# Performance work log

Measured on AMD Instinct MI355X. Metric: run time of the kernel, lower is better.

## Reference

```python
import jax, jax.numpy as jnp
import numpy as np

B, IN, O, F, FH = 512, 2000, 64, 8, 32
D = 64 + FH * O  # 2112


def setup_inputs() -> dict:
    key = jax.random.key(0)
    ks = jax.random.split(key, 17)
    rn = lambda k, s: jax.random.normal(k, s, dtype=jnp.float32) * 0.05
    return dict(
        x=rn(ks[0], (B, IN)),
        fc_in_W=rn(ks[1], (1024, IN)), fc_in_b=rn(ks[2], (1024,)),
        fc1_W=rn(ks[3], (128, 1024)), fc1_b=rn(ks[4], (128,)),
        out1_W=rn(ks[5], (O, 64, 128)), out1_b=rn(ks[6], (O, 64)),
        coef_nn_W=rn(ks[7], (F, FH, 1)), coef_nn_b=rn(ks[8], (F, FH)),
        coef_att_W=rn(ks[9], (F, FH, FH)),
        out_att_W=rn(ks[10], (O, FH, FH)),
        nodes_trans_W=rn(ks[11], (O, O)),
        trans_gcn_W=rn(ks[12], (D, D)),
        outmap_W=rn(ks[13], (1, D)), outmap_b=rn(ks[14], (1,)),
        prelu_a=jnp.float32(0.25),
        coef_m=rn(ks[15], (O, O, F)),
    )


def reference(x, fc_in_W, fc_in_b, fc1_W, fc1_b, out1_W, out1_b,
              coef_nn_W, coef_nn_b, coef_att_W, out_att_W,
              nodes_trans_W, trans_gcn_W, outmap_W, outmap_b, prelu_a, coef_m):
    elu = jax.nn.elu
    # trunk MLP
    h = jax.nn.relu(x @ fc_in_W.T + fc_in_b)          # [B,1024]
    h = jax.nn.relu(h @ fc1_W.T + fc1_b)              # [B,128]
    # per-output-node heads (vectorized over the output_dim loop)
    hiddens = jax.nn.relu(jnp.einsum('bk,odk->bod', h, out1_W) + out1_b)  # [B,O,64]
    # per-feature coef embedding: Linear(1,FH) on each coef_m[:,:,i] slice
    cf = elu(coef_m[..., None] * coef_nn_W[:, :, 0] + coef_nn_b)          # [O,O,F,FH]
    # sum over concatenated feature axis (F*FH) of exp(elu(.))
    s = jnp.exp(elu(cf)).sum(axis=(2, 3))[:, :, None, None]               # [O,O,1,1]
    lin = jnp.einsum('xyfh,fgh->xyfg', cf, coef_att_W)                    # per-feature attention linear
    p = elu(jnp.exp(elu(cf)) * lin / s)
    cfs = elu(p.sum(axis=2) / F)                                          # [O,O,FH]
    # node-level attention (vectorized over the output_dim loop)
    coef_sum = jnp.exp(elu(cfs)).sum(axis=1)                              # [O,FH]
    p2 = jnp.exp(elu(cfs)) / coef_sum[:, None, :]                         # [O,O,FH]
    lin2 = jnp.einsum('oih,igh->oig', cfs, out_att_W)
    att = (p2 * lin2).reshape(O, O * FH)                                  # concat over i (i-major)
    hc = jnp.concatenate(
        [hiddens, jnp.broadcast_to(att[None], (x.shape[0], O, O * FH))], axis=2)  # [B,O,D]
    nt = jnp.einsum('bpd,op->bod', hc, nodes_trans_W)                     # node mixing Linear(O,O)
    trans = jax.nn.sigmoid(jnp.einsum('bod,ed->boe', nt, trans_gcn_W))    # [B,O,D]
    z = (trans @ outmap_W.T + outmap_b).squeeze(-1)                       # [B,O]
    return jnp.where(z >= 0, z, prelu_a * z)                              # PReLU
```

## Files before the change

### kernel.cpp

```cpp
#include <hip/hip_runtime.h>
#include <math.h>

typedef __attribute__((ext_vector_type(8))) short bf16x8;
typedef __attribute__((ext_vector_type(4))) float f32x4;

static __device__ __forceinline__ float fast_elu(float x) {
    return x > 0.0f ? x : __expf(x) - 1.0f;
}

static __device__ __forceinline__ unsigned short f2bf(float f) {
    unsigned int u = __float_as_uint(f);
    unsigned int r = (u + 0x7FFFu + ((u >> 16) & 1u)) >> 16;
    return (unsigned short)r;
}

#define CV0 1048576
#define CV1 3145728
#define CV2 3276800
#define CV3 3280896
#define CV4 3805184
#define CV5 8265728
__global__ __launch_bounds__(256) void conv_all(
    const float* __restrict__ x, const float* __restrict__ fcinW,
    const float* __restrict__ fc1W, const float* __restrict__ ntW,
    const float* __restrict__ out1W, const float* __restrict__ tgw,
    unsigned short* __restrict__ xb, unsigned short* __restrict__ fcinWb,
    unsigned short* __restrict__ fc1Wb, unsigned short* __restrict__ Wb,
    unsigned short* __restrict__ out1WbT,
    unsigned short* __restrict__ Gb, unsigned short* __restrict__ G2b)
{
    int idx = blockIdx.x * 256 + threadIdx.x;
    if (idx < CV0) {
        int r = idx >> 11, k = idx & 2047;
        xb[idx] = (k < 2000) ? f2bf(x[(size_t)r * 2000 + k]) : (unsigned short)0;
    } else if (idx < CV1) {
        int i = idx - CV0;
        int r = i >> 11, k = i & 2047;
        fcinWb[i] = (k < 2000) ? f2bf(fcinW[(size_t)r * 2000 + k]) : (unsigned short)0;
    } else if (idx < CV2) {
        int i = idx - CV1;
        fc1Wb[i] = f2bf(fc1W[i]);
    } else if (idx < CV3) {
        int i = idx - CV2;
        Wb[i] = f2bf(ntW[i]);
    } else if (idx < CV4) {
        int i = idx - CV3;
        int n = i >> 7, k = i & 127, d = n >> 6, p = n & 63;
        out1WbT[i] = f2bf(out1W[(size_t)((p << 6) | d) * 128 + k]);
    } else if (idx < CV5) {
        int i = idx - CV4;
        int e = i / 2112, k = i - e * 2112;
        unsigned short v = f2bf(tgw[(size_t)e * 2112 + k]);
        if (k < 64) Gb[e * 64 + k] = v;
        else        G2b[(size_t)e * 2048 + (k - 64)] = v;
    }
}

__global__ __launch_bounds__(256) void gemm_mfma(
    const unsigned short* __restrict__ A, int lda,
    const unsigned short* __restrict__ B, int ldb,
    float* __restrict__ C, unsigned short* __restrict__ Cb,
    int ldc, long strideCz,
    const float* __restrict__ bias, int mode, int kchunk)
{
    __shared__ __align__(16) unsigned short As[64 * 40];
    __shared__ __align__(16) unsigned short Bs[64 * 40];
    const int t = threadIdx.x;
    const int w = t >> 6, lane = t & 63, l16 = lane & 15, quad = lane >> 4;
    const int n0 = blockIdx.x * 64, m0 = blockIdx.y * 64;
    const int kb0 = blockIdx.z * kchunk;
    const int r = t >> 2, koff = (t & 3) * 8;
    if (mode == 0) C += (size_t)blockIdx.z * strideCz;

    const size_t arow = (size_t)(m0 + r) * lda + koff;
    const size_t brow = (size_t)(n0 + r) * ldb + koff;
    bf16x8 av = *reinterpret_cast<const bf16x8*>(&A[arow + kb0]);
    bf16x8 bv = *reinterpret_cast<const bf16x8*>(&B[brow + kb0]);

    f32x4 acc[4] = {};
    for (int kb = kb0; kb < kb0 + kchunk; kb += 32) {
        __syncthreads();
        *reinterpret_cast<bf16x8*>(&As[r * 40 + koff]) = av;
        *reinterpret_cast<bf16x8*>(&Bs[r * 40 + koff]) = bv;
        if (kb + 32 < kb0 + kchunk) {
            av = *reinterpret_cast<const bf16x8*>(&A[arow + kb + 32]);
            bv = *reinterpret_cast<const bf16x8*>(&B[brow + kb + 32]);
        }
        __syncthreads();
        bf16x8 af = *reinterpret_cast<const bf16x8*>(&As[(w * 16 + l16) * 40 + quad * 8]);
        #pragma unroll
        for (int nt = 0; nt < 4; ++nt) {
            bf16x8 bf = *reinterpret_cast<const bf16x8*>(&Bs[(nt * 16 + l16) * 40 + quad * 8]);
            acc[nt] = __builtin_amdgcn_mfma_f32_16x16x32_bf16(af, bf, acc[nt], 0, 0, 0);
        }
    }
    #pragma unroll
    for (int nt = 0; nt < 4; ++nt)
        #pragma unroll
        for (int i = 0; i < 4; ++i) {
            int m = m0 + w * 16 + quad * 4 + i;
            int n = n0 + nt * 16 + l16;
            if (mode == 0) {
                C[(size_t)m * ldc + n] = acc[nt][i];
            } else {
                int bidx = (((n & 63) << 6) | (n >> 6));
                float v = acc[nt][i] + bias[bidx];
                v = fmaxf(v, 0.0f);
                Cb[(size_t)m * ldc + n] = f2bf(v);
            }
        }
}

__global__ __launch_bounds__(256) void reduce_partials(
    const float* __restrict__ src, float* __restrict__ dstF,
    unsigned short* __restrict__ dstB, int n,
    int nparts, long pstride, const float* __restrict__ bias, int biasMask, int doRelu)
{
    int i = blockIdx.x * 256 + threadIdx.x;
    if (i >= n) return;
    float a = 0.0f;
    for (int j = 0; j < nparts; ++j) a += src[i + (long)j * pstride];
    if (bias) a += bias[i & biasMask];
    if (doRelu) a = fmaxf(a, 0.0f);
    if (dstB) dstB[i] = f2bf(a); else dstF[i] = a;
}

__global__ __launch_bounds__(256) void coef_kernel(
    const float* __restrict__ coef_m,
    const float* __restrict__ cW,
    const float* __restrict__ cB,
    const float* __restrict__ attW,
    float* __restrict__ cfs)
{
    __shared__ float cf_s[4][256];
    __shared__ float part[4][64];
    const int t = threadIdx.x;
    const int wv = t >> 6, lane = t & 63;
    const int xy = blockIdx.x * 4 + wv;
    float ls = 0.0f;
    #pragma unroll
    for (int i = 0; i < 4; ++i) {
        int idx = i * 64 + lane;
        int f = idx >> 5;
        float v = fast_elu(coef_m[xy * 8 + f] * cW[idx] + cB[idx]);
        cf_s[wv][idx] = v;
        ls += __expf(fast_elu(v));
    }
    #pragma unroll
    for (int m = 1; m < 64; m <<= 1) ls += __shfl_xor(ls, m, 64);
    __syncthreads();
    const float rs = __builtin_amdgcn_rcpf(ls);
    const int g = lane & 31, fg = lane >> 5;
    float acc = 0.0f;
    for (int f = fg * 4; f < fg * 4 + 4; ++f) {
        float lin = 0.0f;
        #pragma unroll
        for (int h = 0; h < 32; h += 4) {
            float4 Lv = *reinterpret_cast<const float4*>(&cf_s[wv][f * 32 + h]);
            float4 Wv = *reinterpret_cast<const float4*>(&attW[f * 1024 + g * 32 + h]);
            lin += Lv.x * Wv.x + Lv.y * Wv.y + Lv.z * Wv.z + Lv.w * Wv.w;
        }
        float e = __expf(fast_elu(cf_s[wv][f * 32 + g]));
        acc += fast_elu(e * lin * rs);
    }
    part[wv][lane] = acc;
    __syncthreads();
    if (lane < 32) {
        float tot = part[wv][lane] + part[wv][lane + 32];
        cfs[xy * 32 + lane] = fast_elu(tot * 0.125f);
    }
}

__global__ __launch_bounds__(1024) void att_kernel(
    const float* __restrict__ cfs,
    const float* __restrict__ oattW,
    float* __restrict__ att)
{
    __shared__ float L[2048];
    __shared__ float red[1024];
    __shared__ float csum[32];
    const int t = threadIdx.x;
    const int o = blockIdx.x;
    L[t] = cfs[o * 2048 + t];
    L[t + 1024] = cfs[o * 2048 + 1024 + t];
    __syncthreads();
    {
        int h = t & 31, ig = t >> 5;
        red[t] = __expf(fast_elu(L[(2 * ig) * 32 + h])) +
                 __expf(fast_elu(L[(2 * ig + 1) * 32 + h]));
        __syncthreads();
        if (t < 32) {
            float cs = 0.0f;
            #pragma unroll
            for (int j = 0; j < 32; ++j) cs += red[j * 32 + t];
            csum[t] = cs;
        }
        __syncthreads();
    }
    #pragma unroll
    for (int j = 0; j < 2; ++j) {
        int idx = t + 1024 * j;
        int i = idx >> 5, g = idx & 31;
        float lin2 = 0.0f;
        #pragma unroll
        for (int h = 0; h < 32; h += 4) {
            float4 Lv = *reinterpret_cast<const float4*>(&L[i * 32 + h]);
            float4 Wv = *reinterpret_cast<const float4*>(&oattW[i * 1024 + g * 32 + h]);
            lin2 += Lv.x * Wv.x + Lv.y * Wv.y + Lv.z * Wv.z + Lv.w * Wv.w;
        }
        float p2 = __expf(fast_elu(L[idx])) * __builtin_amdgcn_rcpf(csum[g]);
        att[o * 2048 + idx] = p2 * lin2;
    }
}

__global__ __launch_bounds__(256) void natt_new(
    const float* __restrict__ ntW,
    const float* __restrict__ att,
    unsigned short* __restrict__ nattb)
{
    __shared__ float ntW_s[64 * 65];
    __shared__ float att_s[64 * 17];
    const int t = threadIdx.x;
    const int d0 = blockIdx.x * 16;
    #pragma unroll
    for (int j = 0; j < 16; ++j) {
        int idx = t + 256 * j;
        ntW_s[(idx >> 6) * 65 + (idx & 63)] = ntW[idx];
    }
    #pragma unroll
    for (int j = 0; j < 4; ++j) {
        int idx = t + 256 * j;
        int p = idx >> 4, dd = idx & 15;
        att_s[p * 17 + dd] = att[p * 2048 + d0 + dd];
    }
    __syncthreads();
    const int dd = t & 15, ob = (t >> 4) * 4;
    float acc[4] = {0.0f, 0.0f, 0.0f, 0.0f};
    for (int p = 0; p < 64; ++p) {
        float av = att_s[p * 17 + dd];
        #pragma unroll
        for (int i = 0; i < 4; ++i) acc[i] += ntW_s[(ob + i) * 65 + p] * av;
    }
    #pragma unroll
    for (int i = 0; i < 4; ++i)
        nattb[(ob + i) * 2048 + d0 + dd] = f2bf(acc[i]);
}

__global__ __launch_bounds__(256) void final_part(
    const unsigned short* __restrict__ hbT,
    const unsigned short* __restrict__ Wb,
    const unsigned short* __restrict__ Gb,
    const float* __restrict__ cmatT,
    const float* __restrict__ outW,
    float* __restrict__ zpart)
{
    __shared__ __align__(16) unsigned short HtT[64 * 72];
    __shared__ __align__(16) unsigned short nt1_s[64 * 72];
    __shared__ float zp[4][64];
    const int t = threadIdx.x;
    const int w = t >> 6;
    const int lane = t & 63;
    const int l16 = lane & 15, quad = lane >> 4;
    const int b = blockIdx.x;
    const int z = blockIdx.y;

    const unsigned short* src = hbT + (size_t)b * 4096;
    #pragma unroll
    for (int j = 0; j < 2; ++j) {
        int c = t + j * 256;
        *reinterpret_cast<bf16x8*>(&HtT[(c >> 3) * 72 + (c & 7) * 8]) =
            *reinterpret_cast<const bf16x8*>(&src[c * 8]);
    }
    __syncthreads();

    bf16x8 aW[2];
    #pragma unroll
    for (int h = 0; h < 2; ++h)
        aW[h] = *reinterpret_cast<const bf16x8*>(&Wb[(w * 16 + l16) * 64 + h * 32 + quad * 8]);
    #pragma unroll
    for (int dt = 0; dt < 4; ++dt) {
        f32x4 acc = {0.0f, 0.0f, 0.0f, 0.0f};
        #pragma unroll
        for (int h = 0; h < 2; ++h) {
            bf16x8 bf = *reinterpret_cast<const bf16x8*>(
                &HtT[(dt * 16 + l16) * 72 + h * 32 + quad * 8]);
            acc = __builtin_amdgcn_mfma_f32_16x16x32_bf16(aW[h], bf, acc, 0, 0, 0);
        }
        #pragma unroll
        for (int i = 0; i < 4; ++i)
            nt1_s[(w * 16 + quad * 4 + i) * 72 + dt * 16 + l16] = f2bf(acc[i]);
    }
    __syncthreads();

    bf16x8 afr[4][2];
    #pragma unroll
    for (int ot = 0; ot < 4; ++ot)
        #pragma unroll
        for (int h = 0; h < 2; ++h)
            afr[ot][h] = *reinterpret_cast<const bf16x8*>(
                &nt1_s[(ot * 16 + l16) * 72 + h * 32 + quad * 8]);

    float zacc[4][4] = {};
    int e = z * 64 + w * 16 + l16;
    bf16x8 g0 = *reinterpret_cast<const bf16x8*>(&Gb[(size_t)e * 64 + quad * 8]);
    bf16x8 g1 = *reinterpret_cast<const bf16x8*>(&Gb[(size_t)e * 64 + 32 + quad * 8]);
    float wv = outW[e];
    float4 c4[4];
    #pragma unroll
    for (int ot = 0; ot < 4; ++ot)
        c4[ot] = *reinterpret_cast<const float4*>(&cmatT[(size_t)e * 64 + ot * 16 + quad * 4]);

    for (int ec = z; ec < 33; ec += 4) {
        const int en = e + 256;
        const bool more = (ec + 4 < 33);
        bf16x8 ng0, ng1; float4 nc4[4]; float nwv;
        if (more) {
            ng0 = *reinterpret_cast<const bf16x8*>(&Gb[(size_t)en * 64 + quad * 8]);
            ng1 = *reinterpret_cast<const bf16x8*>(&Gb[(size_t)en * 64 + 32 + quad * 8]);
            nwv = outW[en];
            #pragma unroll
            for (int ot = 0; ot < 4; ++ot)
                nc4[ot] = *reinterpret_cast<const float4*>(
                    &cmatT[(size_t)en * 64 + ot * 16 + quad * 4]);
        }
        #pragma unroll
        for (int ot = 0; ot < 4; ++ot) {
            f32x4 acc = {c4[ot].x, c4[ot].y, c4[ot].z, c4[ot].w};
            acc = __builtin_amdgcn_mfma_f32_16x16x32_bf16(afr[ot][0], g0, acc, 0, 0, 0);
            acc = __builtin_amdgcn_mfma_f32_16x16x32_bf16(afr[ot][1], g1, acc, 0, 0, 0);
            #pragma unroll
            for (int i = 0; i < 4; ++i) {
                float sg = __builtin_amdgcn_rcpf(1.0f + __expf(-acc[i]));
                zacc[ot][i] += sg * wv;
            }
        }
        if (more) {
            g0 = ng0; g1 = ng1; wv = nwv;
            #pragma unroll
            for (int ot = 0; ot < 4; ++ot) c4[ot] = nc4[ot];
        }
        e = en;
    }
    #pragma unroll
    for (int m = 1; m < 16; m <<= 1)
        #pragma unroll
        for (int ot = 0; ot < 4; ++ot)
            #pragma unroll
            for (int i = 0; i < 4; ++i)
                zacc[ot][i] += __shfl_xor(zacc[ot][i], m, 64);

    if (l16 == 0) {
        #pragma unroll
        for (int ot = 0; ot < 4; ++ot)
            #pragma unroll
            for (int i = 0; i < 4; ++i)
                zp[w][ot * 16 + quad * 4 + i] = zacc[ot][i];
    }
    __syncthreads();
    if (t < 64)
        zpart[((size_t)z * 512 + b) * 64 + t] = zp[0][t] + zp[1][t] + zp[2][t] + zp[3][t];
}

__global__ __launch_bounds__(256) void finish_kernel(
    const float* __restrict__ zpart, const float* __restrict__ outB,
    const float* __restrict__ preluA, float* __restrict__ out)
{
    int i = blockIdx.x * 256 + threadIdx.x;
    float z = zpart[i] + zpart[32768 + i] + zpart[65536 + i] + zpart[98304 + i] + outB[0];
    float pa = preluA[0];
    out[i] = (z >= 0.0f) ? z : pa * z;
}

extern "C" void kernel_launch(void* const* d_in, const int* in_sizes, int n_in,
                              void* d_out, int out_size, void* d_ws, size_t ws_size,
                              hipStream_t stream)
{
    const float* x       = (const float*)d_in[0];
    const float* fc_in_W = (const float*)d_in[1];
    const float* fc_in_b = (const float*)d_in[2];
    const float* fc1_W   = (const float*)d_in[3];
    const float* fc1_b   = (const float*)d_in[4];
    const float* out1_W  = (const float*)d_in[5];
    const float* out1_b  = (const float*)d_in[6];
    const float* cW      = (const float*)d_in[7];
    const float* cB      = (const float*)d_in[8];
    const float* cattW   = (const float*)d_in[9];
    const float* oattW   = (const float*)d_in[10];
    const float* ntW     = (const float*)d_in[11];
    const float* tgw     = (const float*)d_in[12];
    const float* outW    = (const float*)d_in[13];
    const float* outB    = (const float*)d_in[14];
    const float* preluA  = (const float*)d_in[15];
    const float* coef_m  = (const float*)d_in[16];
    float* out = (float*)d_out;
    float* ws  = (float*)d_ws;

    unsigned short* xb      = (unsigned short*)(ws + 0);
    unsigned short* fcinWb  = (unsigned short*)(ws + 524288);
    float*          cpT     = ws + 0;
    float*          h1p     = ws + 1572864;
    unsigned short* hbT     = (unsigned short*)(ws + 1572864);
    unsigned short* h1b     = (unsigned short*)(ws + 3670016);
    unsigned short* fc1Wb   = (unsigned short*)(ws + 3932160);
    float*          h2p     = ws + 3997696;
    float*          zpart   = ws + 3997696;
    unsigned short* h2b     = (unsigned short*)(ws + 4521984);
    unsigned short* out1WbT = (unsigned short*)(ws + 4554752);
    unsigned short* Wb      = (unsigned short*)(ws + 4816896);
    unsigned short* Gb      = (unsigned short*)(ws + 4818944);
    unsigned short* G2b     = (unsigned short*)(ws + 4886528);
    float*          cfs     = ws + 7049216;
    float*          att     = ws + 7180288;
    unsigned short* nattb   = (unsigned short*)(ws + 7311360);
    float*          cmatT   = ws + 7376896;

    conv_all<<<(CV5 + 255) / 256, 256, 0, stream>>>(
        x, fc_in_W, fc1_W, ntW, out1_W, tgw,
        xb, fcinWb, fc1Wb, Wb, out1WbT, Gb, G2b);

    coef_kernel<<<1024, 256, 0, stream>>>(coef_m, cW, cB, cattW, cfs);
    att_kernel<<<64, 1024, 0, stream>>>(cfs, oattW, att);
    natt_new<<<128, 256, 0, stream>>>(ntW, att, nattb);

    gemm_mfma<<<dim3(16, 8, 4), 256, 0, stream>>>(xb, 2048, fcinWb, 2048,
        h1p, nullptr, 1024, 524288L, nullptr, 0, 512);
    reduce_partials<<<2048, 256, 0, stream>>>(h1p, nullptr, h1b, 524288, 4,
        524288L, fc_in_b, 1023, 1);
    gemm_mfma<<<dim3(2, 8, 8), 256, 0, stream>>>(h1b, 1024, fc1Wb, 1024,
        h2p, nullptr, 128, 65536L, nullptr, 0, 128);
    reduce_partials<<<256, 256, 0, stream>>>(h2p, nullptr, h2b, 65536, 8,
        65536L, fc1_b, 127, 1);
    gemm_mfma<<<dim3(64, 8, 1), 256, 0, stream>>>(h2b, 128, out1WbT, 128,
        nullptr, hbT, 4096, 0L, out1_b, 2, 128);

    gemm_mfma<<<dim3(1, 33, 8), 256, 0, stream>>>(G2b, 2048, nattb, 2048,
        cpT, nullptr, 64, 135168L, nullptr, 0, 256);
    reduce_partials<<<528, 256, 0, stream>>>(cpT, cmatT, nullptr, 135168, 8,
        135168L, nullptr, 0, 0);

    final_part<<<dim3(512, 4), 256, 0, stream>>>(hbT, Wb, Gb, cmatT, outW, zpart);
    finish_kernel<<<128, 256, 0, stream>>>(zpart, outB, preluA, out);
}
```

Measured before the change: 234.4 us.

## Fuse split-K reductions into GEMM loads, merge coef/att kernels, split final stage

Adds a GEMM variant that sums the split-K partials, adds bias and applies ReLU while loading its A operand. This removes two reduce_partials launches and their intermediate bf16 buffers. The coef and att kernels are merged into one 1024-thread kernel so cfs stays in shared memory. The node-mixing MFMA is moved out of final_part into a separate nt1f kernel, and final_part now runs over 8 z-slices instead of 4, with finish summing 8 partials. The cost is redundant partial-sum reads in each GEMM block, one extra launch plus an nt1b round-trip through global memory, and lower parallelism in the fused coef/att kernel.

```diff
diff --git a/kernel.cpp b/kernel.cpp
--- a/kernel.cpp
+++ b/kernel.cpp
@@ -111,79 +111,138 @@
         }
 }
 
+__global__ __launch_bounds__(256) void gemm_mfma_fa(
+    const float* __restrict__ Ap, int lda, long apstride, int nparts,
+    const float* __restrict__ abias,
+    const unsigned short* __restrict__ B, int ldb,
+    float* __restrict__ C, unsigned short* __restrict__ Cb,
+    int ldc, long strideCz,
+    const float* __restrict__ bias, int mode, int kchunk)
+{
+    __shared__ __align__(16) unsigned short As[64 * 40];
+    __shared__ __align__(16) unsigned short Bs[64 * 40];
+    const int t = threadIdx.x;
+    const int w = t >> 6, lane = t & 63, l16 = lane & 15, quad = lane >> 4;
+    const int n0 = blockIdx.x * 64, m0 = blockIdx.y * 64;
+    const int kb0 = blockIdx.z * kchunk;
+    const int r = t >> 2, koff = (t & 3) * 8;
+    if (mode == 0) C += (size_t)blockIdx.z * strideCz;
+
+    f32x4 acc[4] = {};
+    for (int kb = kb0; kb < kb0 + kchunk; kb += 32) {
+        float a8[8];
+        {
+            const float* base = &Ap[(size_t)(m0 + r) * lda + kb + koff];
+            float4 s0 = *reinterpret_cast<const float4*>(base);
+            float4 s1 = *reinterpret_cast<const float4*>(base + 4);
+            for (int j = 1; j < nparts; ++j) {
+                const float* pj = base + (size_t)j * apstride;
+                float4 p0 = *reinterpret_cast<const float4*>(pj);
+                float4 p1 = *reinterpret_cast<const float4*>(pj + 4);
+                s0.x += p0.x; s0.y += p0.y; s0.z += p0.z; s0.w += p0.w;
+                s1.x += p1.x; s1.y += p1.y; s1.z += p1.z; s1.w += p1.w;
+            }
+            float4 b0 = *reinterpret_cast<const float4*>(&abias[kb + koff]);
+            float4 b1 = *reinterpret_cast<const float4*>(&abias[kb + koff + 4]);
+            a8[0] = fmaxf(s0.x + b0.x, 0.0f); a8[1] = fmaxf(s0.y + b0.y, 0.0f);
+            a8[2] = fmaxf(s0.z + b0.z, 0.0f); a8[3] = fmaxf(s0.w + b0.w, 0.0f);
+            a8[4] = fmaxf(s1.x + b1.x, 0.0f); a8[5] = fmaxf(s1.y + b1.y, 0.0f);
+            a8[6] = fmaxf(s1.z + b1.z, 0.0f); a8[7] = fmaxf(s1.w + b1.w, 0.0f);
+        }
+        bf16x8 bv = *reinterpret_cast<const bf16x8*>(&B[(size_t)(n0 + r) * ldb + kb + koff]);
+        __syncthreads();
+        ushort4 lo, hi;
+        lo.x = f2bf(a8[0]); lo.y = f2bf(a8[1]); lo.z = f2bf(a8[2]); lo.w = f2bf(a8[3]);
+        hi.x = f2bf(a8[4]); hi.y = f2bf(a8[5]); hi.z = f2bf(a8[6]); hi.w = f2bf(a8[7]);
+        *reinterpret_cast<ushort4*>(&As[r * 40 + koff]) = lo;
+        *reinterpret_cast<ushort4*>(&As[r * 40 + koff + 4]) = hi;
+        *reinterpret_cast<bf16x8*>(&Bs[r * 40 + koff]) = bv;
+        __syncthreads();
+        bf16x8 af = *reinterpret_cast<const bf16x8*>(&As[(w * 16 + l16) * 40 + quad * 8]);
+        #pragma unroll
+        for (int nt = 0; nt < 4; ++nt) {
+            bf16x8 bf = *reinterpret_cast<const bf16x8*>(&Bs[(nt * 16 + l16) * 40 + quad * 8]);
+            acc[nt] = __builtin_amdgcn_mfma_f32_16x16x32_bf16(af, bf, acc[nt], 0, 0, 0);
+        }
+    }
+    #pragma unroll
+    for (int nt = 0; nt < 4; ++nt)
+        #pragma unroll
+        for (int i = 0; i < 4; ++i) {
+            int m = m0 + w * 16 + quad * 4 + i;
+            int n = n0 + nt * 16 + l16;
+            if (mode == 0) {
+                C[(size_t)m * ldc + n] = acc[nt][i];
+            } else {
+                int bidx = (((n & 63) << 6) | (n >> 6));
+                float v = acc[nt][i] + bias[bidx];
+                v = fmaxf(v, 0.0f);
+                Cb[(size_t)m * ldc + n] = f2bf(v);
+            }
+        }
+}
+
 __global__ __launch_bounds__(256) void reduce_partials(
-    const float* __restrict__ src, float* __restrict__ dstF,
-    unsigned short* __restrict__ dstB, int n,
-    int nparts, long pstride, const float* __restrict__ bias, int biasMask, int doRelu)
+    const float* __restrict__ src, float* __restrict__ dst, int n,
+    int nparts, long pstride)
 {
     int i = blockIdx.x * 256 + threadIdx.x;
     if (i >= n) return;
     float a = 0.0f;
     for (int j = 0; j < nparts; ++j) a += src[i + (long)j * pstride];
-    if (bias) a += bias[i & biasMask];
-    if (doRelu) a = fmaxf(a, 0.0f);
-    if (dstB) dstB[i] = f2bf(a); else dstF[i] = a;
-}
-
-__global__ __launch_bounds__(256) void coef_kernel(
+    dst[i] = a;
+}
+
+__global__ __launch_bounds__(1024) void coef_att(
     const float* __restrict__ coef_m,
     const float* __restrict__ cW,
     const float* __restrict__ cB,
     const float* __restrict__ attW,
-    float* __restrict__ cfs)
-{
-    __shared__ float cf_s[4][256];
-    __shared__ float part[4][64];
-    const int t = threadIdx.x;
-    const int wv = t >> 6, lane = t & 63;
-    const int xy = blockIdx.x * 4 + wv;
-    float ls = 0.0f;
-    #pragma unroll
-    for (int i = 0; i < 4; ++i) {
-        int idx = i * 64 + lane;
-        int f = idx >> 5;
-        float v = fast_elu(coef_m[xy * 8 + f] * cW[idx] + cB[idx]);
-        cf_s[wv][idx] = v;
-        ls += __expf(fast_elu(v));
-    }
-    #pragma unroll
-    for (int m = 1; m < 64; m <<= 1) ls += __shfl_xor(ls, m, 64);
-    __syncthreads();
-    const float rs = __builtin_amdgcn_rcpf(ls);
-    const int g = lane & 31, fg = lane >> 5;
-    float acc = 0.0f;
-    for (int f = fg * 4; f < fg * 4 + 4; ++f) {
-        float lin = 0.0f;
-        #pragma unroll
-        for (int h = 0; h < 32; h += 4) {
-            float4 Lv = *reinterpret_cast<const float4*>(&cf_s[wv][f * 32 + h]);
-            float4 Wv = *reinterpret_cast<const float4*>(&attW[f * 1024 + g * 32 + h]);
-            lin += Lv.x * Wv.x + Lv.y * Wv.y + Lv.z * Wv.z + Lv.w * Wv.w;
-        }
-        float e = __expf(fast_elu(cf_s[wv][f * 32 + g]));
-        acc += fast_elu(e * lin * rs);
-    }
-    part[wv][lane] = acc;
-    __syncthreads();
-    if (lane < 32) {
-        float tot = part[wv][lane] + part[wv][lane + 32];
-        cfs[xy * 32 + lane] = fast_elu(tot * 0.125f);
-    }
-}
-
-__global__ __launch_bounds__(1024) void att_kernel(
-    const float* __restrict__ cfs,
     const float* __restrict__ oattW,
     float* __restrict__ att)
 {
     __shared__ float L[2048];
     __shared__ float red[1024];
     __shared__ float csum[32];
+    __shared__ float cf_s[16][256];
     const int t = threadIdx.x;
-    const int o = blockIdx.x;
-    L[t] = cfs[o * 2048 + t];
-    L[t + 1024] = cfs[o * 2048 + 1024 + t];
+    const int wv = t >> 6, lane = t & 63;
+    const int x = blockIdx.x;
+
+    #pragma unroll
+    for (int q = 0; q < 4; ++q) {
+        const int y = wv * 4 + q;
+        const int xy = x * 64 + y;
+        float ls = 0.0f;
+        #pragma unroll
+        for (int i = 0; i < 4; ++i) {
+            int idx = i * 64 + lane;
+            int f = idx >> 5;
+            float v = fast_elu(coef_m[xy * 8 + f] * cW[idx] + cB[idx]);
+            cf_s[wv][idx] = v;
+            ls += __expf(fast_elu(v));
+        }
+        #pragma unroll
+        for (int m = 1; m < 64; m <<= 1) ls += __shfl_xor(ls, m, 64);
+        const float rs = __builtin_amdgcn_rcpf(ls);
+        const int g = lane & 31, fg = lane >> 5;
+        float acc = 0.0f;
+        for (int f = fg * 4; f < fg * 4 + 4; ++f) {
+            float lin = 0.0f;
+            #pragma unroll
+            for (int h = 0; h < 32; h += 4) {
+                float4 Lv = *reinterpret_cast<const float4*>(&cf_s[wv][f * 32 + h]);
+                float4 Wv = *reinterpret_cast<const float4*>(&attW[f * 1024 + g * 32 + h]);
+                lin += Lv.x * Wv.x + Lv.y * Wv.y + Lv.z * Wv.z + Lv.w * Wv.w;
+            }
+            float e = __expf(fast_elu(cf_s[wv][f * 32 + g]));
+            acc += fast_elu(e * lin * rs);
+        }
+        acc += __shfl_xor(acc, 32, 64);
+        if (fg == 0) L[y * 32 + g] = fast_elu(acc * 0.125f);
+    }
     __syncthreads();
+
     {
         int h = t & 31, ig = t >> 5;
         red[t] = __expf(fast_elu(L[(2 * ig) * 32 + h])) +
@@ -209,7 +268,7 @@
             lin2 += Lv.x * Wv.x + Lv.y * Wv.y + Lv.z * Wv.z + Lv.w * Wv.w;
         }
         float p2 = __expf(fast_elu(L[idx])) * __builtin_amdgcn_rcpf(csum[g]);
-        att[o * 2048 + idx] = p2 * lin2;
+        att[x * 2048 + idx] = p2 * lin2;
     }
 }
 
@@ -246,16 +305,59 @@
         nattb[(ob + i) * 2048 + d0 + dd] = f2bf(acc[i]);
 }
 
-__global__ __launch_bounds__(256) void final_part(
+__global__ __launch_bounds__(256) void nt1f(
     const unsigned short* __restrict__ hbT,
     const unsigned short* __restrict__ Wb,
+    unsigned short* __restrict__ nt1b)
+{
+    __shared__ __align__(16) unsigned short HtT[64 * 72];
+    __shared__ __align__(16) unsigned short nt1_s[64 * 72];
+    const int t = threadIdx.x;
+    const int w = t >> 6, lane = t & 63, l16 = lane & 15, quad = lane >> 4;
+    const int b = blockIdx.x;
+
+    const unsigned short* src = hbT + (size_t)b * 4096;
+    #pragma unroll
+    for (int j = 0; j < 2; ++j) {
+        int c = t + j * 256;
+        *reinterpret_cast<bf16x8*>(&HtT[(c >> 3) * 72 + (c & 7) * 8]) =
+            *reinterpret_cast<const bf16x8*>(&src[c * 8]);
+    }
+    __syncthreads();
+
+    bf16x8 aW[2];
+    #pragma unroll
+    for (int h = 0; h < 2; ++h)
+        aW[h] = *reinterpret_cast<const bf16x8*>(&Wb[(w * 16 + l16) * 64 + h * 32 + quad * 8]);
+    #pragma unroll
+    for (int dt = 0; dt < 4; ++dt) {
+        f32x4 acc = {0.0f, 0.0f, 0.0f, 0.0f};
+        #pragma unroll
+        for (int h = 0; h < 2; ++h) {
+            bf16x8 bf = *reinterpret_cast<const bf16x8*>(
+                &HtT[(dt * 16 + l16) * 72 + h * 32 + quad * 8]);
+            acc = __builtin_amdgcn_mfma_f32_16x16x32_bf16(aW[h], bf, acc, 0, 0, 0);
+        }
+        #pragma unroll
+        for (int i = 0; i < 4; ++i)
+            nt1_s[(w * 16 + quad * 4 + i) * 72 + dt * 16 + l16] = f2bf(acc[i]);
+    }
+    __syncthreads();
+    #pragma unroll
+    for (int j = 0; j < 2; ++j) {
+        int c = t + j * 256;
+        *reinterpret_cast<bf16x8*>(&nt1b[(size_t)b * 4096 + c * 8]) =
+            *reinterpret_cast<const bf16x8*>(&nt1_s[(c >> 3) * 72 + (c & 7) * 8]);
+    }
+}
+
+__global__ __launch_bounds__(256) void final_part(
+    const unsigned short* __restrict__ nt1b,
     const unsigned short* __restrict__ Gb,
     const float* __restrict__ cmatT,
     const float* __restrict__ outW,
     float* __restrict__ zpart)
 {
-    __shared__ __align__(16) unsigned short HtT[64 * 72];
-    __shared__ __align__(16) unsigned short nt1_s[64 * 72];
     __shared__ float zp[4][64];
     const int t = threadIdx.x;
     const int w = t >> 6;
@@ -264,41 +366,14 @@
     const int b = blockIdx.x;
     const int z = blockIdx.y;
 
-    const unsigned short* src = hbT + (size_t)b * 4096;
-    #pragma unroll
-    for (int j = 0; j < 2; ++j) {
-        int c = t + j * 256;
-        *reinterpret_cast<bf16x8*>(&HtT[(c >> 3) * 72 + (c & 7) * 8]) =
-            *reinterpret_cast<const bf16x8*>(&src[c * 8]);
-    }
-    __syncthreads();
-
-    bf16x8 aW[2];
-    #pragma unroll
-    for (int h = 0; h < 2; ++h)
-        aW[h] = *reinterpret_cast<const bf16x8*>(&Wb[(w * 16 + l16) * 64 + h * 32 + quad * 8]);
-    #pragma unroll
-    for (int dt = 0; dt < 4; ++dt) {
-        f32x4 acc = {0.0f, 0.0f, 0.0f, 0.0f};
-        #pragma unroll
-        for (int h = 0; h < 2; ++h) {
-            bf16x8 bf = *reinterpret_cast<const bf16x8*>(
-                &HtT[(dt * 16 + l16) * 72 + h * 32 + quad * 8]);
-            acc = __builtin_amdgcn_mfma_f32_16x16x32_bf16(aW[h], bf, acc, 0, 0, 0);
-        }
-        #pragma unroll
-        for (int i = 0; i < 4; ++i)
-            nt1_s[(w * 16 + quad * 4 + i) * 72 + dt * 16 + l16] = f2bf(acc[i]);
-    }
-    __syncthreads();
-
     bf16x8 afr[4][2];
+    const unsigned short* Abase = nt1b + (size_t)b * 4096;
     #pragma unroll
     for (int ot = 0; ot < 4; ++ot)
         #pragma unroll
         for (int h = 0; h < 2; ++h)
             afr[ot][h] = *reinterpret_cast<const bf16x8*>(
-                &nt1_s[(ot * 16 + l16) * 72 + h * 32 + quad * 8]);
+                &Abase[(ot * 16 + l16) * 64 + h * 32 + quad * 8]);
 
     float zacc[4][4] = {};
     int e = z * 64 + w * 16 + l16;
@@ -310,9 +385,9 @@
     for (int ot = 0; ot < 4; ++ot)
         c4[ot] = *reinterpret_cast<const float4*>(&cmatT[(size_t)e * 64 + ot * 16 + quad * 4]);
 
-    for (int ec = z; ec < 33; ec += 4) {
-        const int en = e + 256;
-        const bool more = (ec + 4 < 33);
+    for (int ec = z; ec < 33; ec += 8) {
+        const int en = e + 512;
+        const bool more = (ec + 8 < 33);
         bf16x8 ng0, ng1; float4 nc4[4]; float nwv;
         if (more) {
             ng0 = *reinterpret_cast<const bf16x8*>(&Gb[(size_t)en * 64 + quad * 8]);
@@ -366,7 +441,10 @@
     const float* __restrict__ preluA, float* __restrict__ out)
 {
     int i = blockIdx.x * 256 + threadIdx.x;
-    float z = zpart[i] + zpart[32768 + i] + zpart[65536 + i] + zpart[98304 + i] + outB[0];
+    float z = 0.0f;
+    #pragma unroll
+    for (int j = 0; j < 8; ++j) z += zpart[j * 32768 + i];
+    z += outB[0];
     float pa = preluA[0];
     out[i] = (z >= 0.0f) ? z : pa * z;
 }
@@ -399,45 +477,38 @@
     unsigned short* fcinWb  = (unsigned short*)(ws + 524288);
     float*          cpT     = ws + 0;
     float*          h1p     = ws + 1572864;
-    unsigned short* hbT     = (unsigned short*)(ws + 1572864);
-    unsigned short* h1b     = (unsigned short*)(ws + 3670016);
-    unsigned short* fc1Wb   = (unsigned short*)(ws + 3932160);
-    float*          h2p     = ws + 3997696;
-    float*          zpart   = ws + 3997696;
-    unsigned short* h2b     = (unsigned short*)(ws + 4521984);
-    unsigned short* out1WbT = (unsigned short*)(ws + 4554752);
-    unsigned short* Wb      = (unsigned short*)(ws + 4816896);
-    unsigned short* Gb      = (unsigned short*)(ws + 4818944);
-    unsigned short* G2b     = (unsigned short*)(ws + 4886528);
-    float*          cfs     = ws + 7049216;
-    float*          att     = ws + 7180288;
-    unsigned short* nattb   = (unsigned short*)(ws + 7311360);
-    float*          cmatT   = ws + 7376896;
+    unsigned short* nt1b    = (unsigned short*)(ws + 1572864);
+    float*          zpart   = ws + 2621440;
+    unsigned short* fc1Wb   = (unsigned short*)(ws + 3670016);
+    float*          h2p     = ws + 3735552;
+    unsigned short* out1WbT = (unsigned short*)(ws + 3997696);
+    unsigned short* hbT     = (unsigned short*)(ws + 4259840);
+    unsigned short* Wb      = (unsigned short*)(ws + 5308416);
+    unsigned short* Gb      = (unsigned short*)(ws + 5310464);
+    unsigned short* G2b     = (unsigned short*)(ws + 5378048);
+    float*          att     = ws + 7540736;
+    unsigned short* nattb   = (unsigned short*)(ws + 7671808);
+    float*          cmatT   = ws + 7737344;
 
     conv_all<<<(CV5 + 255) / 256, 256, 0, stream>>>(
         x, fc_in_W, fc1_W, ntW, out1_W, tgw,
         xb, fcinWb, fc1Wb, Wb, out1WbT, Gb, G2b);
 
-    coef_kernel<<<1024, 256, 0, stream>>>(coef_m, cW, cB, cattW, cfs);
-    att_kernel<<<64, 1024, 0, stream>>>(cfs, oattW, att);
+    coef_att<<<64, 1024, 0, stream>>>(coef_m, cW, cB, cattW, oattW, att);
     natt_new<<<128, 256, 0, stream>>>(ntW, att, nattb);
 
     gemm_mfma<<<dim3(16, 8, 4), 256, 0, stream>>>(xb, 2048, fcinWb, 2048,
         h1p, nullptr, 1024, 524288L, nullptr, 0, 512);
-    reduce_partials<<<2048, 256, 0, stream>>>(h1p, nullptr, h1b, 524288, 4,
-        524288L, fc_in_b, 1023, 1);
-    gemm_mfma<<<dim3(2, 8, 8), 256, 0, stream>>>(h1b, 1024, fc1Wb, 1024,
-        h2p, nullptr, 128, 65536L, nullptr, 0, 128);
-    reduce_partials<<<256, 256, 0, stream>>>(h2p, nullptr, h2b, 65536, 8,
-        65536L, fc1_b, 127, 1);
-    gemm_mfma<<<dim3(64, 8, 1), 256, 0, stream>>>(h2b, 128, out1WbT, 128,
-        nullptr, hbT, 4096, 0L, out1_b, 2, 128);
+    gemm_mfma_fa<<<dim3(2, 8, 4), 256, 0, stream>>>(h1p, 1024, 524288L, 4,
+        fc_in_b, fc1Wb, 1024, h2p, nullptr, 128, 65536L, nullptr, 0, 256);
+    gemm_mfma_fa<<<dim3(64, 8, 1), 256, 0, stream>>>(h2p, 128, 65536L, 4,
+        fc1_b, out1WbT, 128, nullptr, hbT, 4096, 0L, out1_b, 2, 128);
 
     gemm_mfma<<<dim3(1, 33, 8), 256, 0, stream>>>(G2b, 2048, nattb, 2048,
         cpT, nullptr, 64, 135168L, nullptr, 0, 256);
-    reduce_partials<<<528, 256, 0, stream>>>(cpT, cmatT, nullptr, 135168, 8,
-        135168L, nullptr, 0, 0);
-
-    final_part<<<dim3(512, 4), 256, 0, stream>>>(hbT, Wb, Gb, cmatT, outW, zpart);
+    reduce_partials<<<528, 256, 0, stream>>>(cpT, cmatT, 135168, 8, 135168L);
+
+    nt1f<<<512, 256, 0, stream>>>(hbT, Wb, nt1b);
+    final_part<<<dim3(512, 8), 256, 0, stream>>>(nt1b, Gb, cmatT, outW, zpart);
     finish_kernel<<<128, 256, 0, stream>>>(zpart, outB, preluA, out);
 }
```

Result: slower. 296.2 us (+26.4%).
